# Kernel tuning notes

Hardware: AMD Instinct MI355X
Metric: run time of the kernel (lower is better)

Reference implementation:

```python
import jax, jax.numpy as jnp
import numpy as np

N = 10000      # nodes
E = 160000     # edges
IN = 512       # in_feat
H = 512        # hidden_dim
L = 6          # layers
C = 64         # num_class
EPS = 1e-5     # BatchNorm eps


def setup_inputs() -> dict:
    key = jax.random.key(0)
    ks = jax.random.split(key, 12)
    x = jax.random.normal(ks[0], (N, IN), jnp.float32)
    src = jax.random.randint(ks[1], (E,), 0, N)
    dst = jax.random.randint(ks[2], (E,), 0, N)
    W0 = jax.random.normal(ks[3], (IN, H), jnp.float32) * (1.0 / np.sqrt(IN))
    Ws = jax.random.normal(ks[4], (L - 1, H, H), jnp.float32) * (1.0 / np.sqrt(H))
    bs = jnp.zeros((L, H), jnp.float32)
    gamma = jnp.ones((L, H), jnp.float32) + 0.1 * jax.random.normal(ks[5], (L, H), jnp.float32)
    beta = 0.1 * jax.random.normal(ks[6], (L, H), jnp.float32)
    run_mean = 0.1 * jax.random.normal(ks[7], (L, H), jnp.float32)
    run_var = jax.random.uniform(ks[8], (L, H), jnp.float32, 0.5, 1.5)
    linW = jax.random.normal(ks[9], (L * H, C), jnp.float32) * (1.0 / np.sqrt(L * H))
    linb = jnp.zeros((C,), jnp.float32)
    return {"x": x, "W0": W0, "Ws": Ws, "bs": bs, "gamma": gamma, "beta": beta,
            "run_mean": run_mean, "run_var": run_var, "linW": linW, "linb": linb,
            "src": src, "dst": dst}


def reference(x, W0, Ws, bs, gamma, beta, run_mean, run_var, linW, linb, src, dst):
    ones_e = jnp.ones((E,), jnp.float32)
    out_deg = jax.ops.segment_sum(ones_e, src, num_segments=N)
    in_deg = jax.ops.segment_sum(ones_e, dst, num_segments=N)
    # DGL GraphConv norm='both': D_dst^{-1/2} A D_src^{-1/2}, zero-deg clamped to 1
    norm_src = jnp.clip(out_deg, 1.0, None) ** -0.5   # [N]
    norm_dst = jnp.clip(in_deg, 1.0, None) ** -0.5    # [N]

    h = x
    hs = []
    for i in range(L):
        W = W0 if i == 0 else Ws[i - 1]
        m = (h * norm_src[:, None]) @ W                 # [N, H] GEMM
        agg = jax.ops.segment_sum(m[src], dst, num_segments=N)  # gather/scatter
        h = agg * norm_dst[:, None] + bs[i]
        # BatchNorm1d (inference, running stats) + ReLU; dropout is identity in eval
        scale = gamma[i] * jax.lax.rsqrt(run_var[i] + EPS)
        h = jax.nn.relu((h - run_mean[i]) * scale + beta[i])
        hs.append(h)
    h = jnp.concatenate(hs, axis=-1)                    # [N, L*H] JK-concat
    return h @ linW + linb                              # [N, C]
```

## Files before the change

### kernel.cpp

```cpp
#include <hip/hip_runtime.h>

#define NN 10000
#define NNPAD 10112
#define NE 160000
#define HF 512
#define LL 6
#define NC 64
#define KCAT (LL*HF)
#define BN_EPS 1e-5f

typedef _Float16 f16x8 __attribute__((ext_vector_type(8)));
typedef _Float16 f16x4 __attribute__((ext_vector_type(4)));
typedef float f32x4 __attribute__((ext_vector_type(4)));

#define GLB(p) ((const __attribute__((address_space(1))) void*)(p))
#define LDSP(p) ((__attribute__((address_space(3))) void*)(p))


__global__ void zero_u32_kernel(unsigned* __restrict__ p, int n) {
  int i = blockIdx.x * blockDim.x + threadIdx.x;
  if (i < n) p[i] = 0u;
}

__global__ void deg_kernel(const int* __restrict__ src, const int* __restrict__ dst,
                           unsigned* __restrict__ cnt_out, unsigned* __restrict__ cnt_in) {
  int e = blockIdx.x * blockDim.x + threadIdx.x;
  if (e < NE) {
    atomicAdd(&cnt_out[src[e]], 1u);
    atomicAdd(&cnt_in[dst[e]], 1u);
  }
}

__global__ void prep_kernel(const unsigned* __restrict__ cnt_out, const unsigned* __restrict__ cnt_in,
                            float* __restrict__ norm_src, float* __restrict__ norm_dst,
                            const float* __restrict__ bs, const float* __restrict__ gamma,
                            const float* __restrict__ beta, const float* __restrict__ rmean,
                            const float* __restrict__ rvar,
                            float* __restrict__ scale, float* __restrict__ shift) {
  int i = blockIdx.x * blockDim.x + threadIdx.x;
  if (i < NN) {
    unsigned co = cnt_out[i]; if (co < 1u) co = 1u;
    unsigned ci = cnt_in[i];  if (ci < 1u) ci = 1u;
    norm_src[i] = rsqrtf((float)co);
    norm_dst[i] = rsqrtf((float)ci);
  }
  if (i < LL * HF) {
    float s = gamma[i] * rsqrtf(rvar[i] + BN_EPS);
    scale[i] = s;
    shift[i] = (bs[i] - rmean[i]) * s + beta[i];
  }
}

__global__ void scan_kernel(const unsigned* __restrict__ cnt, unsigned* __restrict__ off) {
  __shared__ unsigned wsum[16];
  int tid = threadIdx.x;
  int lane = tid & 63, wid = tid >> 6;
  unsigned base = 0;
  for (int c = 0; c < NN; c += 1024) {
    int i = c + tid;
    unsigned v = (i < NN) ? cnt[i] : 0u;
    unsigned x = v;
    #pragma unroll
    for (int d = 1; d < 64; d <<= 1) {
      unsigned y = __shfl_up(x, d, 64);
      if (lane >= d) x += y;
    }
    if (lane == 63) wsum[wid] = x;
    __syncthreads();
    if (wid == 0 && lane < 16) {
      unsigned s = wsum[lane];
      #pragma unroll
      for (int d = 1; d < 16; d <<= 1) {
        unsigned y = __shfl_up(s, d, 16);
        if (lane >= d) s += y;
      }
      wsum[lane] = s;
    }
    __syncthreads();
    unsigned wbase = wid ? wsum[wid - 1] : 0u;
    if (i < NN) off[i] = base + wbase + x - v;
    unsigned tot = wsum[15];
    __syncthreads();
    base += tot;
  }
  if (tid == 0) off[NN] = base;
}

__global__ void fill_kernel(const int* __restrict__ src, const int* __restrict__ dst,
                            const unsigned* __restrict__ off, unsigned* __restrict__ cursor,
                            int* __restrict__ edge_src) {
  int e = blockIdx.x * blockDim.x + threadIdx.x;
  if (e < NE) {
    int d = dst[e];
    unsigned p = atomicAdd(&cursor[d], 1u);
    edge_src[off[d] + p] = src[e];
  }
}

__global__ void convert_w(const float* __restrict__ W0, const float* __restrict__ Ws,
                          _Float16* __restrict__ Wt) {
  int l = blockIdx.z;
  const float* W = (l == 0) ? W0 : (Ws + (size_t)(l - 1) * HF * HF);
  __shared__ float t[32][33];
  int n0 = blockIdx.x * 32, k0 = blockIdx.y * 32;
  int tx = threadIdx.x & 31, ty4 = (threadIdx.x >> 5) * 4;
  #pragma unroll
  for (int j = 0; j < 4; ++j)
    t[ty4 + j][tx] = W[(size_t)(k0 + ty4 + j) * HF + n0 + tx];
  __syncthreads();
  size_t base = (size_t)l * HF * HF;
  #pragma unroll
  for (int j = 0; j < 4; ++j)
    Wt[base + (size_t)(n0 + ty4 + j) * HF + k0 + tx] = (_Float16)t[tx][ty4 + j];
}

__global__ void convert_lin(const float* __restrict__ linW, _Float16* __restrict__ Lt) {
  __shared__ float t[32][33];
  int n0 = blockIdx.x * 32, k0 = blockIdx.y * 32;
  int tx = threadIdx.x & 31, ty4 = (threadIdx.x >> 5) * 4;
  #pragma unroll
  for (int j = 0; j < 4; ++j)
    t[ty4 + j][tx] = linW[(size_t)(k0 + ty4 + j) * NC + n0 + tx];
  __syncthreads();
  #pragma unroll
  for (int j = 0; j < 4; ++j)
    Lt[(size_t)(n0 + ty4 + j) * KCAT + k0 + tx] = (_Float16)t[tx][ty4 + j];
}

__global__ void split_x(const float* __restrict__ x, _Float16* __restrict__ zh) {
  int i = blockIdx.x * blockDim.x + threadIdx.x;
  if (i >= NN * HF / 4) return;
  int base = i * 4;
  float4 v = *(const float4*)&x[base];
  f16x4 h;
  h.x = (_Float16)v.x;
  h.y = (_Float16)v.y;
  h.z = (_Float16)v.z;
  h.w = (_Float16)v.w;
  *(f16x4*)&zh[base] = h;
}

__launch_bounds__(256, 2)
__global__ void gemm_layer_f16(const _Float16* __restrict__ Z, int lda,
                               const _Float16* __restrict__ Wt,
                               _Float16* __restrict__ Mout) {
  __shared__ _Float16 As[128][64];
  __shared__ _Float16 Bs[128][64];
  int m0 = blockIdx.y * 128;
  int n0 = blockIdx.x * 128;
  int wid = threadIdx.x >> 6, lane = threadIdx.x & 63;
  int wr = wid >> 1, wc = wid & 1;
  int fr = lane & 15, kg = lane >> 4;
  int rr = lane >> 3;
  int ck = (lane & 7) ^ rr;

  f32x4 acc[4][4];
  #pragma unroll
  for (int m = 0; m < 4; ++m)
    #pragma unroll
    for (int n = 0; n < 4; ++n)
      acc[m][n] = (f32x4){0.f, 0.f, 0.f, 0.f};

  const _Float16* gA = Z  + (size_t)(m0 + wid * 32 + rr) * lda + ck * 8;
  const _Float16* gB = Wt + (size_t)(n0 + wid * 32 + rr) * HF + ck * 8;

  for (int k0 = 0; k0 < HF; k0 += 64) {
    __syncthreads();
    #pragma unroll
    for (int i = 0; i < 4; ++i) {
      __builtin_amdgcn_global_load_lds(GLB(gA + (size_t)i * 8 * lda + k0),
                                       LDSP(&As[wid * 32 + i * 8][0]), 16, 0, 0);
      __builtin_amdgcn_global_load_lds(GLB(gB + (size_t)i * 8 * HF + k0),
                                       LDSP(&Bs[wid * 32 + i * 8][0]), 16, 0, 0);
    }
    __syncthreads();
    #pragma unroll
    for (int kk = 0; kk < 2; ++kk) {
      f16x8 a[4], b[4];
      #pragma unroll
      for (int n = 0; n < 4; ++n) {
        int row = wc * 64 + n * 16 + fr;
        b[n] = *(const f16x8*)&Bs[row][((kk * 4 + kg) ^ (row & 7)) * 8];
      }
      #pragma unroll
      for (int m = 0; m < 4; ++m) {
        int row = wr * 64 + m * 16 + fr;
        a[m] = *(const f16x8*)&As[row][((kk * 4 + kg) ^ (row & 7)) * 8];
      }
      #pragma unroll
      for (int m = 0; m < 4; ++m)
        #pragma unroll
        for (int n = 0; n < 4; ++n)
          acc[m][n] = __builtin_amdgcn_mfma_f32_16x16x32_f16(a[m], b[n], acc[m][n], 0, 0, 0);
    }
  }
  #pragma unroll
  for (int m = 0; m < 4; ++m) {
    #pragma unroll
    for (int j = 0; j < 4; ++j) {
      int row = m0 + wr * 64 + m * 16 + kg * 4 + j;
      if (row < NN) {
        #pragma unroll
        for (int n = 0; n < 4; ++n) {
          int col = n0 + wc * 64 + n * 16 + fr;
          Mout[(size_t)row * HF + col] = (_Float16)acc[m][n][j];
        }
      }
    }
  }
}

__launch_bounds__(256)
__global__ void agg_bn_kernel(const _Float16* __restrict__ Mm,
                              const int* __restrict__ edge_src,
                              const unsigned* __restrict__ row_off,
                              const float* __restrict__ norm_dst,
                              const float* __restrict__ norm_src,
                              const float* __restrict__ bn_scale,
                              const float* __restrict__ bn_shift,
                              _Float16* __restrict__ hcat_col) {
  int n = blockIdx.x * 4 + (threadIdx.x >> 6);
  if (n >= NN) return;
  int f = (threadIdx.x & 63) * 8;
  unsigned e0 = row_off[n], e1 = row_off[n + 1];
  float a0=0.f,a1=0.f,a2=0.f,a3=0.f,a4=0.f,a5=0.f,a6=0.f,a7=0.f;
  unsigned e = e0;
  for (; e + 4 <= e1; e += 4) {
    int s0 = edge_src[e], s1 = edge_src[e + 1], s2 = edge_src[e + 2], s3 = edge_src[e + 3];
    float n0 = norm_src[s0], n1 = norm_src[s1], n2 = norm_src[s2], n3 = norm_src[s3];
    f16x8 v0 = *(const f16x8*)&Mm[(size_t)s0 * HF + f];
    f16x8 v1 = *(const f16x8*)&Mm[(size_t)s1 * HF + f];
    f16x8 v2 = *(const f16x8*)&Mm[(size_t)s2 * HF + f];
    f16x8 v3 = *(const f16x8*)&Mm[(size_t)s3 * HF + f];
    a0 = fmaf((float)v0[0], n0, fmaf((float)v1[0], n1, fmaf((float)v2[0], n2, fmaf((float)v3[0], n3, a0))));
    a1 = fmaf((float)v0[1], n0, fmaf((float)v1[1], n1, fmaf((float)v2[1], n2, fmaf((float)v3[1], n3, a1))));
    a2 = fmaf((float)v0[2], n0, fmaf((float)v1[2], n1, fmaf((float)v2[2], n2, fmaf((float)v3[2], n3, a2))));
    a3 = fmaf((float)v0[3], n0, fmaf((float)v1[3], n1, fmaf((float)v2[3], n2, fmaf((float)v3[3], n3, a3))));
    a4 = fmaf((float)v0[4], n0, fmaf((float)v1[4], n1, fmaf((float)v2[4], n2, fmaf((float)v3[4], n3, a4))));
    a5 = fmaf((float)v0[5], n0, fmaf((float)v1[5], n1, fmaf((float)v2[5], n2, fmaf((float)v3[5], n3, a5))));
    a6 = fmaf((float)v0[6], n0, fmaf((float)v1[6], n1, fmaf((float)v2[6], n2, fmaf((float)v3[6], n3, a6))));
    a7 = fmaf((float)v0[7], n0, fmaf((float)v1[7], n1, fmaf((float)v2[7], n2, fmaf((float)v3[7], n3, a7))));
  }
  for (; e < e1; ++e) {
    int s = edge_src[e];
    float ns = norm_src[s];
    f16x8 v = *(const f16x8*)&Mm[(size_t)s * HF + f];
    a0 = fmaf((float)v[0], ns, a0); a1 = fmaf((float)v[1], ns, a1);
    a2 = fmaf((float)v[2], ns, a2); a3 = fmaf((float)v[3], ns, a3);
    a4 = fmaf((float)v[4], ns, a4); a5 = fmaf((float)v[5], ns, a5);
    a6 = fmaf((float)v[6], ns, a6); a7 = fmaf((float)v[7], ns, a7);
  }
  float nd = norm_dst[n];
  float4 s0 = *(const float4*)&bn_scale[f];
  float4 s1 = *(const float4*)&bn_scale[f + 4];
  float4 t0 = *(const float4*)&bn_shift[f];
  float4 t1 = *(const float4*)&bn_shift[f + 4];
  float y0 = fmaxf(fmaf(a0 * nd, s0.x, t0.x), 0.f);
  float y1 = fmaxf(fmaf(a1 * nd, s0.y, t0.y), 0.f);
  float y2 = fmaxf(fmaf(a2 * nd, s0.z, t0.z), 0.f);
  float y3 = fmaxf(fmaf(a3 * nd, s0.w, t0.w), 0.f);
  float y4 = fmaxf(fmaf(a4 * nd, s1.x, t1.x), 0.f);
  float y5 = fmaxf(fmaf(a5 * nd, s1.y, t1.y), 0.f);
  float y6 = fmaxf(fmaf(a6 * nd, s1.z, t1.z), 0.f);
  float y7 = fmaxf(fmaf(a7 * nd, s1.w, t1.w), 0.f);
  f16x8 hv;
  hv[0]=(_Float16)y0; hv[1]=(_Float16)y1; hv[2]=(_Float16)y2; hv[3]=(_Float16)y3;
  hv[4]=(_Float16)y4; hv[5]=(_Float16)y5; hv[6]=(_Float16)y6; hv[7]=(_Float16)y7;
  *(f16x8*)&hcat_col[(size_t)n * KCAT + f] = hv;
}

__launch_bounds__(256, 2)
__global__ void final_gemm_f16(const _Float16* __restrict__ Hc,
                               const _Float16* __restrict__ Lt,
                               float* __restrict__ part) {
  __shared__ _Float16 As[128][64];
  __shared__ _Float16 Bs[64][64];
  int m0 = blockIdx.x * 128;
  int sp = blockIdx.y;
  int kbase = sp * HF;
  int wid = threadIdx.x >> 6, lane = threadIdx.x & 63;
  int fr = lane & 15, kg = lane >> 4;
  int rr = lane >> 3;
  int ck = (lane & 7) ^ rr;

  f32x4 acc[2][4];
  #pragma unroll
  for (int m = 0; m < 2; ++m)
    #pragma unroll
    for (int n = 0; n < 4; ++n)
      acc[m][n] = (f32x4){0.f, 0.f, 0.f, 0.f};

  const _Float16* gA = Hc + (size_t)(m0 + wid * 32 + rr) * KCAT + kbase + ck * 8;
  const _Float16* gB = Lt + (size_t)(wid * 16 + rr) * KCAT + kbase + ck * 8;

  for (int k0 = 0; k0 < HF; k0 += 64) {
    __syncthreads();
    #pragma unroll
    for (int i = 0; i < 4; ++i)
      __builtin_amdgcn_global_load_lds(GLB(gA + (size_t)i * 8 * KCAT + k0),
                                       LDSP(&As[wid * 32 + i * 8][0]), 16, 0, 0);
    #pragma unroll
    for (int i = 0; i < 2; ++i)
      __builtin_amdgcn_global_load_lds(GLB(gB + (size_t)i * 8 * KCAT + k0),
                                       LDSP(&Bs[wid * 16 + i * 8][0]), 16, 0, 0);
    __syncthreads();
    #pragma unroll
    for (int kk = 0; kk < 2; ++kk) {
      f16x8 a[2], b[4];
      #pragma unroll
      for (int n = 0; n < 4; ++n) {
        int row = n * 16 + fr;
        b[n] = *(const f16x8*)&Bs[row][((kk * 4 + kg) ^ (row & 7)) * 8];
      }
      #pragma unroll
      for (int m = 0; m < 2; ++m) {
        int row = wid * 32 + m * 16 + fr;
        a[m] = *(const f16x8*)&As[row][((kk * 4 + kg) ^ (row & 7)) * 8];
      }
      #pragma unroll
      for (int m = 0; m < 2; ++m)
        #pragma unroll
        for (int n = 0; n < 4; ++n)
          acc[m][n] = __builtin_amdgcn_mfma_f32_16x16x32_f16(a[m], b[n], acc[m][n], 0, 0, 0);
    }
  }
  #pragma unroll
  for (int m = 0; m < 2; ++m) {
    #pragma unroll
    for (int j = 0; j < 4; ++j) {
      int row = m0 + wid * 32 + m * 16 + kg * 4 + j;
      if (row < NN) {
        #pragma unroll
        for (int n = 0; n < 4; ++n) {
          int col = n * 16 + fr;
          part[((size_t)sp * NN + row) * NC + col] = acc[m][n][j];
        }
      }
    }
  }
}

__launch_bounds__(256)
__global__ void final_reduce(const float* __restrict__ part,
                             const float* __restrict__ linb,
                             float* __restrict__ out) {
  int i = blockIdx.x * blockDim.x + threadIdx.x;
  if (i >= NN * NC / 4) return;
  int n  = i >> 4;
  int cq = i & 15;
  float4 s = *(const float4*)&linb[cq * 4];
  #pragma unroll
  for (int sp = 0; sp < LL; ++sp) {
    float4 v = *(const float4*)&part[((size_t)sp * NN + n) * NC + cq * 4];
    s.x += v.x; s.y += v.y; s.z += v.z; s.w += v.w;
  }
  *(float4*)&out[(size_t)n * NC + cq * 4] = s;
}


extern "C" void kernel_launch(void* const* d_in, const int* in_sizes, int n_in,
                              void* d_out, int out_size, void* d_ws, size_t ws_size,
                              hipStream_t stream) {
  const float* x     = (const float*)d_in[0];
  const float* W0    = (const float*)d_in[1];
  const float* Ws    = (const float*)d_in[2];
  const float* bs    = (const float*)d_in[3];
  const float* gamma = (const float*)d_in[4];
  const float* beta  = (const float*)d_in[5];
  const float* rmean = (const float*)d_in[6];
  const float* rvar  = (const float*)d_in[7];
  const float* linW  = (const float*)d_in[8];
  const float* linb  = (const float*)d_in[9];
  const int*   src   = (const int*)d_in[10];
  const int*   dst   = (const int*)d_in[11];
  float* out = (float*)d_out;

  char* w = (char*)d_ws;
  size_t o = 0;
  auto carve = [&](size_t bytes) -> void* {
    o = (o + 255) & ~(size_t)255;
    void* p = w + o;
    o += bytes;
    return p;
  };
  _Float16*  m_buf = (_Float16*)carve((size_t)NNPAD * HF * 2);
  _Float16*  hcat  = (_Float16*)carve((size_t)NNPAD * KCAT * 2);
  _Float16*  zh    = (_Float16*)carve((size_t)NNPAD * HF * 2);
  _Float16*  wt    = (_Float16*)carve((size_t)LL * HF * HF * 2);
  _Float16*  lt    = (_Float16*)carve((size_t)NC * KCAT * 2);
  float*     part  = (float*)carve((size_t)LL * NN * NC * 4);
  float*     bnsc  = (float*)carve((size_t)LL * HF * 4);
  float*     bnsh  = (float*)carve((size_t)LL * HF * 4);
  float*     nsrc  = (float*)carve((size_t)NN * 4);
  float*     ndst  = (float*)carve((size_t)NN * 4);
  unsigned*  cnts  = (unsigned*)carve((size_t)3 * NN * 4);
  unsigned*  roff  = (unsigned*)carve((size_t)(NN + 1) * 4);
  int*       esrc  = (int*)carve((size_t)NE * 4);

  unsigned* cnt_out = cnts;
  unsigned* cnt_in  = cnts + NN;
  unsigned* cursor  = cnts + 2 * NN;

  zero_u32_kernel<<<(3 * NN + 255) / 256, 256, 0, stream>>>(cnts, 3 * NN);
  deg_kernel<<<(NE + 255) / 256, 256, 0, stream>>>(src, dst, cnt_out, cnt_in);
  prep_kernel<<<(NN + 255) / 256, 256, 0, stream>>>(cnt_out, cnt_in, nsrc, ndst,
                                                    bs, gamma, beta, rmean, rvar, bnsc, bnsh);
  scan_kernel<<<1, 1024, 0, stream>>>(cnt_in, roff);
  fill_kernel<<<(NE + 255) / 256, 256, 0, stream>>>(src, dst, roff, cursor, esrc);
  convert_w<<<dim3(16, 16, 6), 256, 0, stream>>>(W0, Ws, wt);
  convert_lin<<<dim3(2, 96), 256, 0, stream>>>(linW, lt);
  split_x<<<(NN * HF / 4 + 255) / 256, 256, 0, stream>>>(x, zh);

  for (int l = 0; l < LL; ++l) {
    const _Float16* A   = (l == 0) ? zh : (hcat + (size_t)(l - 1) * HF);
    int             lda = (l == 0) ? HF : KCAT;
    gemm_layer_f16<<<dim3(HF / 128, NNPAD / 128), 256, 0, stream>>>(
        A, lda, wt + (size_t)l * HF * HF, m_buf);
    agg_bn_kernel<<<(NN + 3) / 4, 256, 0, stream>>>(m_buf, esrc, roff, ndst, nsrc,
                                                    bnsc + l * HF, bnsh + l * HF,
                                                    hcat + (size_t)l * HF);
  }
  final_gemm_f16<<<dim3(NNPAD / 128, LL), 256, 0, stream>>>(hcat, lt, part);
  final_reduce<<<(NN * NC / 4 + 255) / 256, 256, 0, stream>>>(part, linb, out);
}
```

Measured before the change: 285.0 us.

## Fold source-norm scaling into layer GEMM epilogue and shrink GEMM M-tile

Moves the per-source-node norm multiplication out of the edge aggregation loop and into the layer GEMM epilogue, so aggregation no longer gathers norm_src per edge. The layer GEMM tile height drops from 128 to 64 rows, occupancy is raised to 3 blocks per CU, and a 1D grid with a remapped block index (strided by 8, apparently for XCD placement) replaces the 2D grid. The aim is more blocks to fill the GPU and fewer random loads during aggregation, at the cost of less reuse of each loaded B tile per block.

```diff
diff --git a/kernel.cpp b/kernel.cpp
--- a/kernel.cpp
+++ b/kernel.cpp
@@ -140,70 +140,76 @@
   *(f16x4*)&zh[base] = h;
 }
 
-__launch_bounds__(256, 2)
+__launch_bounds__(256, 3)
 __global__ void gemm_layer_f16(const _Float16* __restrict__ Z, int lda,
                                const _Float16* __restrict__ Wt,
+                               const float* __restrict__ nsrc,
                                _Float16* __restrict__ Mout) {
-  __shared__ _Float16 As[128][64];
+  __shared__ _Float16 As[64][64];
   __shared__ _Float16 Bs[128][64];
-  int m0 = blockIdx.y * 128;
-  int n0 = blockIdx.x * 128;
+  int bid = blockIdx.x;
+  int wgid = (bid & 7) * 79 + (bid >> 3);
+  int my = wgid >> 2, nx = wgid & 3;
+  int m0 = my * 64;
+  int n0 = nx * 128;
   int wid = threadIdx.x >> 6, lane = threadIdx.x & 63;
   int wr = wid >> 1, wc = wid & 1;
   int fr = lane & 15, kg = lane >> 4;
   int rr = lane >> 3;
   int ck = (lane & 7) ^ rr;
 
-  f32x4 acc[4][4];
-  #pragma unroll
-  for (int m = 0; m < 4; ++m)
+  f32x4 acc[2][4];
+  #pragma unroll
+  for (int m = 0; m < 2; ++m)
     #pragma unroll
     for (int n = 0; n < 4; ++n)
       acc[m][n] = (f32x4){0.f, 0.f, 0.f, 0.f};
 
-  const _Float16* gA = Z  + (size_t)(m0 + wid * 32 + rr) * lda + ck * 8;
+  const _Float16* gA = Z  + (size_t)(m0 + wid * 16 + rr) * lda + ck * 8;
   const _Float16* gB = Wt + (size_t)(n0 + wid * 32 + rr) * HF + ck * 8;
 
   for (int k0 = 0; k0 < HF; k0 += 64) {
     __syncthreads();
     #pragma unroll
-    for (int i = 0; i < 4; ++i) {
+    for (int i = 0; i < 2; ++i)
       __builtin_amdgcn_global_load_lds(GLB(gA + (size_t)i * 8 * lda + k0),
-                                       LDSP(&As[wid * 32 + i * 8][0]), 16, 0, 0);
+                                       LDSP(&As[wid * 16 + i * 8][0]), 16, 0, 0);
+    #pragma unroll
+    for (int i = 0; i < 4; ++i)
       __builtin_amdgcn_global_load_lds(GLB(gB + (size_t)i * 8 * HF + k0),
                                        LDSP(&Bs[wid * 32 + i * 8][0]), 16, 0, 0);
-    }
     __syncthreads();
     #pragma unroll
     for (int kk = 0; kk < 2; ++kk) {
-      f16x8 a[4], b[4];
+      f16x8 a[2], b[4];
       #pragma unroll
       for (int n = 0; n < 4; ++n) {
         int row = wc * 64 + n * 16 + fr;
         b[n] = *(const f16x8*)&Bs[row][((kk * 4 + kg) ^ (row & 7)) * 8];
       }
       #pragma unroll
-      for (int m = 0; m < 4; ++m) {
-        int row = wr * 64 + m * 16 + fr;
+      for (int m = 0; m < 2; ++m) {
+        int row = wr * 32 + m * 16 + fr;
         a[m] = *(const f16x8*)&As[row][((kk * 4 + kg) ^ (row & 7)) * 8];
       }
       #pragma unroll
-      for (int m = 0; m < 4; ++m)
+      for (int m = 0; m < 2; ++m)
         #pragma unroll
         for (int n = 0; n < 4; ++n)
           acc[m][n] = __builtin_amdgcn_mfma_f32_16x16x32_f16(a[m], b[n], acc[m][n], 0, 0, 0);
     }
   }
   #pragma unroll
-  for (int m = 0; m < 4; ++m) {
+  for (int m = 0; m < 2; ++m) {
     #pragma unroll
     for (int j = 0; j < 4; ++j) {
-      int row = m0 + wr * 64 + m * 16 + kg * 4 + j;
+      int row = m0 + wr * 32 + m * 16 + kg * 4 + j;
       if (row < NN) {
+        float s = nsrc[row];
         #pragma unroll
         for (int n = 0; n < 4; ++n) {
           int col = n0 + wc * 64 + n * 16 + fr;
-          Mout[(size_t)row * HF + col] = (_Float16)acc[m][n][j];
+          Mout[(size_t)row * HF + col] = (_Float16)(acc[m][n][j] * s);
         }
       }
     }
@@ -215,7 +221,6 @@
                               const int* __restrict__ edge_src,
                               const unsigned* __restrict__ row_off,
                               const float* __restrict__ norm_dst,
-                              const float* __restrict__ norm_src,
                               const float* __restrict__ bn_scale,
                               const float* __restrict__ bn_shift,
                               _Float16* __restrict__ hcat_col) {
@@ -227,28 +232,24 @@
   unsigned e = e0;
   for (; e + 4 <= e1; e += 4) {
     int s0 = edge_src[e], s1 = edge_src[e + 1], s2 = edge_src[e + 2], s3 = edge_src[e + 3];
-    float n0 = norm_src[s0], n1 = norm_src[s1], n2 = norm_src[s2], n3 = norm_src[s3];
     f16x8 v0 = *(const f16x8*)&Mm[(size_t)s0 * HF + f];
     f16x8 v1 = *(const f16x8*)&Mm[(size_t)s1 * HF + f];
     f16x8 v2 = *(const f16x8*)&Mm[(size_t)s2 * HF + f];
     f16x8 v3 = *(const f16x8*)&Mm[(size_t)s3 * HF + f];
-    a0 = fmaf((float)v0[0], n0, fmaf((float)v1[0], n1, fmaf((float)v2[0], n2, fmaf((float)v3[0], n3, a0))));
-    a1 = fmaf((float)v0[1], n0, fmaf((float)v1[1], n1, fmaf((float)v2[1], n2, fmaf((float)v3[1], n3, a1))));
-    a2 = fmaf((float)v0[2], n0, fmaf((float)v1[2], n1, fmaf((float)v2[2], n2, fmaf((float)v3[2], n3, a2))));
-    a3 = fmaf((float)v0[3], n0, fmaf((float)v1[3], n1, fmaf((float)v2[3], n2, fmaf((float)v3[3], n3, a3))));
-    a4 = fmaf((float)v0[4], n0, fmaf((float)v1[4], n1, fmaf((float)v2[4], n2, fmaf((float)v3[4], n3, a4))));
-    a5 = fmaf((float)v0[5], n0, fmaf((float)v1[5], n1, fmaf((float)v2[5], n2, fmaf((float)v3[5], n3, a5))));
-    a6 = fmaf((float)v0[6], n0, fmaf((float)v1[6], n1, fmaf((float)v2[6], n2, fmaf((float)v3[6], n3, a6))));
-    a7 = fmaf((float)v0[7], n0, fmaf((float)v1[7], n1, fmaf((float)v2[7], n2, fmaf((float)v3[7], n3, a7))));
+    a0 += (float)v0[0]+(float)v1[0]+(float)v2[0]+(float)v3[0];
+    a1 += (float)v0[1]+(float)v1[1]+(float)v2[1]+(float)v3[1];
+    a2 += (float)v0[2]+(float)v1[2]+(float)v2[2]+(float)v3[2];
+    a3 += (float)v0[3]+(float)v1[3]+(float)v2[3]+(float)v3[3];
+    a4 += (float)v0[4]+(float)v1[4]+(float)v2[4]+(float)v3[4];
+    a5 += (float)v0[5]+(float)v1[5]+(float)v2[5]+(float)v3[5];
+    a6 += (float)v0[6]+(float)v1[6]+(float)v2[6]+(float)v3[6];
+    a7 += (float)v0[7]+(float)v1[7]+(float)v2[7]+(float)v3[7];
   }
   for (; e < e1; ++e) {
     int s = edge_src[e];
-    float ns = norm_src[s];
     f16x8 v = *(const f16x8*)&Mm[(size_t)s * HF + f];
-    a0 = fmaf((float)v[0], ns, a0); a1 = fmaf((float)v[1], ns, a1);
-    a2 = fmaf((float)v[2], ns, a2); a3 = fmaf((float)v[3], ns, a3);
-    a4 = fmaf((float)v[4], ns, a4); a5 = fmaf((float)v[5], ns, a5);
-    a6 = fmaf((float)v[6], ns, a6); a7 = fmaf((float)v[7], ns, a7);
+    a0 += (float)v[0]; a1 += (float)v[1]; a2 += (float)v[2]; a3 += (float)v[3];
+    a4 += (float)v[4]; a5 += (float)v[5]; a6 += (float)v[6]; a7 += (float)v[7];
   }
   float nd = norm_dst[n];
   float4 s0 = *(const float4*)&bn_scale[f];
@@ -414,9 +415,8 @@
   for (int l = 0; l < LL; ++l) {
     const _Float16* A   = (l == 0) ? zh : (hcat + (size_t)(l - 1) * HF);
     int             lda = (l == 0) ? HF : KCAT;
-    gemm_layer_f16<<<dim3(HF / 128, NNPAD / 128), 256, 0, stream>>>(
-        A, lda, wt + (size_t)l * HF * HF, m_buf);
-    agg_bn_kernel<<<(NN + 3) / 4, 256, 0, stream>>>(m_buf, esrc, roff, ndst, nsrc,
+    gemm_layer_f16<<<632, 256, 0, stream>>>(A, lda, wt + (size_t)l * HF * HF, nsrc, m_buf);
+    agg_bn_kernel<<<(NN + 3) / 4, 256, 0, stream>>>(m_buf, esrc, roff, ndst,
                                                     bnsc + l * HF, bnsh + l * HF,
                                                     hcat + (size_t)l * HF);
   }
```

After: 288.5 us. Within noise of the previous version (+1.2%).

## Fold source norm into GEMM epilogue, re-tile aggregation, halve final-GEMM split

Applied to the files above, without the earlier changes.

The per-source degree normalisation now multiplies the GEMM output in its epilogue, so the aggregation kernel only sums gathered rows and no longer loads norm_src per edge. The aggregation kernel is re-mapped so each block covers 16 nodes over one 128-feature chunk, with block index interleaving intended to improve gather locality in L2. The final GEMM K split drops from 6 to 3, giving fewer partial buffers and less reduce traffic at the cost of fewer blocks in that GEMM. Rounding changes slightly because the scale is applied before the fp16 store.

```diff
diff --git a/kernel.cpp b/kernel.cpp
--- a/kernel.cpp
+++ b/kernel.cpp
@@ -8,6 +8,7 @@
 #define NC 64
 #define KCAT (LL*HF)
 #define BN_EPS 1e-5f
+#define FSPLIT 3
 
 typedef _Float16 f16x8 __attribute__((ext_vector_type(8)));
 typedef _Float16 f16x4 __attribute__((ext_vector_type(4)));
@@ -143,6 +144,7 @@
 __launch_bounds__(256, 2)
 __global__ void gemm_layer_f16(const _Float16* __restrict__ Z, int lda,
                                const _Float16* __restrict__ Wt,
+                               const float* __restrict__ nsrc,
                                _Float16* __restrict__ Mout) {
   __shared__ _Float16 As[128][64];
   __shared__ _Float16 Bs[128][64];
@@ -200,10 +202,11 @@
     for (int j = 0; j < 4; ++j) {
       int row = m0 + wr * 64 + m * 16 + kg * 4 + j;
       if (row < NN) {
+        float s = nsrc[row];
         #pragma unroll
         for (int n = 0; n < 4; ++n) {
           int col = n0 + wc * 64 + n * 16 + fr;
-          Mout[(size_t)row * HF + col] = (_Float16)acc[m][n][j];
+          Mout[(size_t)row * HF + col] = (_Float16)(acc[m][n][j] * s);
         }
       }
     }
@@ -215,40 +218,40 @@
                               const int* __restrict__ edge_src,
                               const unsigned* __restrict__ row_off,
                               const float* __restrict__ norm_dst,
-                              const float* __restrict__ norm_src,
                               const float* __restrict__ bn_scale,
                               const float* __restrict__ bn_shift,
                               _Float16* __restrict__ hcat_col) {
-  int n = blockIdx.x * 4 + (threadIdx.x >> 6);
+  int s     = blockIdx.x & 7;
+  int chunk = s >> 1;
+  int grp   = blockIdx.x >> 3;
+  int wave  = threadIdx.x >> 6;
+  int sub   = (threadIdx.x >> 4) & 3;
+  int n = grp * 32 + (s & 1) * 16 + wave * 4 + sub;
   if (n >= NN) return;
-  int f = (threadIdx.x & 63) * 8;
+  int f = chunk * 128 + (threadIdx.x & 15) * 8;
   unsigned e0 = row_off[n], e1 = row_off[n + 1];
   float a0=0.f,a1=0.f,a2=0.f,a3=0.f,a4=0.f,a5=0.f,a6=0.f,a7=0.f;
   unsigned e = e0;
   for (; e + 4 <= e1; e += 4) {
     int s0 = edge_src[e], s1 = edge_src[e + 1], s2 = edge_src[e + 2], s3 = edge_src[e + 3];
-    float n0 = norm_src[s0], n1 = norm_src[s1], n2 = norm_src[s2], n3 = norm_src[s3];
     f16x8 v0 = *(const f16x8*)&Mm[(size_t)s0 * HF + f];
     f16x8 v1 = *(const f16x8*)&Mm[(size_t)s1 * HF + f];
     f16x8 v2 = *(const f16x8*)&Mm[(size_t)s2 * HF + f];
     f16x8 v3 = *(const f16x8*)&Mm[(size_t)s3 * HF + f];
-    a0 = fmaf((float)v0[0], n0, fmaf((float)v1[0], n1, fmaf((float)v2[0], n2, fmaf((float)v3[0], n3, a0))));
-    a1 = fmaf((float)v0[1], n0, fmaf((float)v1[1], n1, fmaf((float)v2[1], n2, fmaf((float)v3[1], n3, a1))));
-    a2 = fmaf((float)v0[2], n0, fmaf((float)v1[2], n1, fmaf((float)v2[2], n2, fmaf((float)v3[2], n3, a2))));
-    a3 = fmaf((float)v0[3], n0, fmaf((float)v1[3], n1, fmaf((float)v2[3], n2, fmaf((float)v3[3], n3, a3))));
-    a4 = fmaf((float)v0[4], n0, fmaf((float)v1[4], n1, fmaf((float)v2[4], n2, fmaf((float)v3[4], n3, a4))));
-    a5 = fmaf((float)v0[5], n0, fmaf((float)v1[5], n1, fmaf((float)v2[5], n2, fmaf((float)v3[5], n3, a5))));
-    a6 = fmaf((float)v0[6], n0, fmaf((float)v1[6], n1, fmaf((float)v2[6], n2, fmaf((float)v3[6], n3, a6))));
-    a7 = fmaf((float)v0[7], n0, fmaf((float)v1[7], n1, fmaf((float)v2[7], n2, fmaf((float)v3[7], n3, a7))));
+    a0 += (float)v0[0]+(float)v1[0]+(float)v2[0]+(float)v3[0];
+    a1 += (float)v0[1]+(float)v1[1]+(float)v2[1]+(float)v3[1];
+    a2 += (float)v0[2]+(float)v1[2]+(float)v2[2]+(float)v3[2];
+    a3 += (float)v0[3]+(float)v1[3]+(float)v2[3]+(float)v3[3];
+    a4 += (float)v0[4]+(float)v1[4]+(float)v2[4]+(float)v3[4];
+    a5 += (float)v0[5]+(float)v1[5]+(float)v2[5]+(float)v3[5];
+    a6 += (float)v0[6]+(float)v1[6]+(float)v2[6]+(float)v3[6];
+    a7 += (float)v0[7]+(float)v1[7]+(float)v2[7]+(float)v3[7];
   }
   for (; e < e1; ++e) {
-    int s = edge_src[e];
-    float ns = norm_src[s];
-    f16x8 v = *(const f16x8*)&Mm[(size_t)s * HF + f];
-    a0 = fmaf((float)v[0], ns, a0); a1 = fmaf((float)v[1], ns, a1);
-    a2 = fmaf((float)v[2], ns, a2); a3 = fmaf((float)v[3], ns, a3);
-    a4 = fmaf((float)v[4], ns, a4); a5 = fmaf((float)v[5], ns, a5);
-    a6 = fmaf((float)v[6], ns, a6); a7 = fmaf((float)v[7], ns, a7);
+    int sx = edge_src[e];
+    f16x8 v = *(const f16x8*)&Mm[(size_t)sx * HF + f];
+    a0 += (float)v[0]; a1 += (float)v[1]; a2 += (float)v[2]; a3 += (float)v[3];
+    a4 += (float)v[4]; a5 += (float)v[5]; a6 += (float)v[6]; a7 += (float)v[7];
   }
   float nd = norm_dst[n];
   float4 s0 = *(const float4*)&bn_scale[f];
@@ -277,7 +280,7 @@
   __shared__ _Float16 Bs[64][64];
   int m0 = blockIdx.x * 128;
   int sp = blockIdx.y;
-  int kbase = sp * HF;
+  int kbase = sp * (KCAT / FSPLIT);
   int wid = threadIdx.x >> 6, lane = threadIdx.x & 63;
   int fr = lane & 15, kg = lane >> 4;
   int rr = lane >> 3;
@@ -293,7 +296,7 @@
   const _Float16* gA = Hc + (size_t)(m0 + wid * 32 + rr) * KCAT + kbase + ck * 8;
   const _Float16* gB = Lt + (size_t)(wid * 16 + rr) * KCAT + kbase + ck * 8;
 
-  for (int k0 = 0; k0 < HF; k0 += 64) {
+  for (int k0 = 0; k0 < KCAT / FSPLIT; k0 += 64) {
     __syncthreads();
     #pragma unroll
     for (int i = 0; i < 4; ++i)
@@ -350,7 +353,7 @@
   int cq = i & 15;
   float4 s = *(const float4*)&linb[cq * 4];
   #pragma unroll
-  for (int sp = 0; sp < LL; ++sp) {
+  for (int sp = 0; sp < FSPLIT; ++sp) {
     float4 v = *(const float4*)&part[((size_t)sp * NN + n) * NC + cq * 4];
     s.x += v.x; s.y += v.y; s.z += v.z; s.w += v.w;
   }
@@ -388,7 +391,7 @@
   _Float16*  zh    = (_Float16*)carve((size_t)NNPAD * HF * 2);
   _Float16*  wt    = (_Float16*)carve((size_t)LL * HF * HF * 2);
   _Float16*  lt    = (_Float16*)carve((size_t)NC * KCAT * 2);
-  float*     part  = (float*)carve((size_t)LL * NN * NC * 4);
+  float*     part  = (float*)carve((size_t)FSPLIT * NN * NC * 4);
   float*     bnsc  = (float*)carve((size_t)LL * HF * 4);
   float*     bnsh  = (float*)carve((size_t)LL * HF * 4);
   float*     nsrc  = (float*)carve((size_t)NN * 4);
@@ -411,15 +414,16 @@
   convert_lin<<<dim3(2, 96), 256, 0, stream>>>(linW, lt);
   split_x<<<(NN * HF / 4 + 255) / 256, 256, 0, stream>>>(x, zh);
 
+  int agg_blocks = ((NN + 31) / 32) * 8;
   for (int l = 0; l < LL; ++l) {
     const _Float16* A   = (l == 0) ? zh : (hcat + (size_t)(l - 1) * HF);
     int             lda = (l == 0) ? HF : KCAT;
     gemm_layer_f16<<<dim3(HF / 128, NNPAD / 128), 256, 0, stream>>>(
-        A, lda, wt + (size_t)l * HF * HF, m_buf);
-    agg_bn_kernel<<<(NN + 3) / 4, 256, 0, stream>>>(m_buf, esrc, roff, ndst, nsrc,
-                                                    bnsc + l * HF, bnsh + l * HF,
-                                                    hcat + (size_t)l * HF);
-  }
-  final_gemm_f16<<<dim3(NNPAD / 128, LL), 256, 0, stream>>>(hcat, lt, part);
+        A, lda, wt + (size_t)l * HF * HF, nsrc, m_buf);
+    agg_bn_kernel<<<agg_blocks, 256, 0, stream>>>(m_buf, esrc, roff, ndst,
+                                                  bnsc + l * HF, bnsh + l * HF,
+                                                  hcat + (size_t)l * HF);
+  }
+  final_gemm_f16<<<dim3(NNPAD / 128, FSPLIT), 256, 0, stream>>>(hcat, lt, part);
   final_reduce<<<(NN * NC / 4 + 255) / 256, 256, 0, stream>>>(part, linb, out);
 }
```

Result: faster. 276.9 us (-2.9%).
